# Optimization experiments

Hardware: AMD Instinct MI355X
Metric: run time of the kernel (lower is better)

The kernel has to match this reference:

```python
import jax, jax.numpy as jnp
import numpy as np

EPS = 1e-5
NUM_GRAPHS = 512


def _glorot(key, shape):
    lim = float(np.sqrt(6.0 / (shape[0] + shape[1])))
    return jax.random.uniform(key, shape, jnp.float32, -lim, lim)


def setup_inputs() -> dict:
    key = jax.random.key(0)
    ks = jax.random.split(key, 20)
    N, E, F0 = 50000, 800000, 64
    x = jax.random.normal(ks[0], (N, F0), jnp.float32)
    edge_index = jax.random.randint(ks[1], (2, E), 0, N, jnp.int64)
    batch = jnp.sort(jax.random.randint(ks[2], (N,), 0, NUM_GRAPHS, jnp.int64))
    dims = [(F0, 128), (128, 64), (64, 32)]
    p = {}
    for i, (di, do) in enumerate(dims, start=1):
        p[f"W{i}l"] = _glorot(ks[3 * i], (di, do))
        p[f"b{i}"] = jnp.zeros((do,), jnp.float32)
        p[f"W{i}r"] = _glorot(ks[3 * i + 1], (di, do))
        p[f"g{i}"] = jnp.ones((do,), jnp.float32)
        p[f"be{i}"] = jnp.zeros((do,), jnp.float32)
    p["Wf1"] = _glorot(ks[13], (32, 128)); p["bf1"] = jnp.zeros((128,), jnp.float32)
    p["Wf2"] = _glorot(ks[14], (128, 64)); p["bf2"] = jnp.zeros((64,), jnp.float32)
    p["Wf3"] = _glorot(ks[15], (64, 2)); p["bf3"] = jnp.zeros((2,), jnp.float32)
    return {"x": x, "edge_index": edge_index, "batch": batch, **p}


def _sage(x, src, dst, Wl, bl, Wr, n):
    # mean-aggregate neighbor features (gather from src, scatter-mean to dst)
    agg = jax.ops.segment_sum(x[src], dst, num_segments=n)
    cnt = jax.ops.segment_sum(jnp.ones((src.shape[0],), x.dtype), dst, num_segments=n)
    mean = agg / jnp.maximum(cnt, 1.0)[:, None]
    return mean @ Wl + bl + x @ Wr


def _bn(x, g, b):
    mu = jnp.mean(x, axis=0)
    var = jnp.mean((x - mu) ** 2, axis=0)  # biased var, torch training mode
    return (x - mu) * jax.lax.rsqrt(var + EPS) * g + b


def reference(x, edge_index, batch,
              W1l, b1, W1r, g1, be1,
              W2l, b2, W2r, g2, be2,
              W3l, b3, W3r, g3, be3,
              Wf1, bf1, Wf2, bf2, Wf3, bf3):
    n = x.shape[0]
    src, dst = edge_index[0], edge_index[1]
    h = _bn(jax.nn.relu(_sage(x, src, dst, W1l, b1, W1r, n)), g1, be1)
    h = _bn(jax.nn.relu(_sage(h, src, dst, W2l, b2, W2r, n)), g2, be2)
    h = _bn(jax.nn.relu(_sage(h, src, dst, W3l, b3, W3r, n)), g3, be3)
    pooled = jax.ops.segment_sum(h, batch, num_segments=NUM_GRAPHS)  # [G, 32]
    cr = jax.nn.relu(pooled @ Wf1 + bf1)  # dropout = identity (eval)
    cr = jax.nn.relu(cr @ Wf2 + bf2)
    cr = cr @ Wf3 + bf3
    return cr.reshape(-1, 2)
```

## Files before the change

### kernel.cpp

```cpp
#include <hip/hip_runtime.h>
#include <hip/hip_bf16.h>

#define EPSBN 1e-5f
#define NGRAPH 512
#define SCAN_NB 128
#define NXCD 8

typedef __attribute__((ext_vector_type(8))) short bf16x8;
typedef __attribute__((ext_vector_type(4))) float f32x4;

__device__ inline short f2bf(float f) {
    unsigned u = __builtin_bit_cast(unsigned, f);
    u += 0x7fffu + ((u >> 16) & 1u);
    return (short)(u >> 16);
}
__device__ inline float bf2f(short s) {
    unsigned u = ((unsigned)(unsigned short)s) << 16;
    return __builtin_bit_cast(float, u);
}

__global__ void __launch_bounds__(256) k_hist(
    const int* __restrict__ dst, int* __restrict__ hist, int E)
{
    for (int e = blockIdx.x * 256 + threadIdx.x; e < E; e += gridDim.x * 256)
        atomicAdd(&hist[dst[e]], 1);
}

__global__ void __launch_bounds__(256) k_scan1(
    const int* __restrict__ hist, int* __restrict__ blocksum, int N)
{
    __shared__ int red[256];
    const int C = (N + SCAN_NB - 1) / SCAN_NB;
    const int b = blockIdx.x, t = threadIdx.x;
    const int lo = b * C, hi = min(lo + C, N);
    int s = 0;
    for (int i = lo + t; i < hi; i += 256) s += hist[i];
    red[t] = s;
    __syncthreads();
    for (int off = 128; off; off >>= 1) {
        if (t < off) red[t] += red[t + off];
        __syncthreads();
    }
    if (t == 0) blocksum[b] = red[0];
}

__global__ void __launch_bounds__(SCAN_NB) k_scan2(
    const int* __restrict__ blocksum, int* __restrict__ blockoff,
    int* __restrict__ row_off, int N)
{
    __shared__ int tmp[SCAN_NB];
    const int t = threadIdx.x;
    int v = blocksum[t];
    tmp[t] = v;
    __syncthreads();
    for (int off = 1; off < SCAN_NB; off <<= 1) {
        int u = (t >= off) ? tmp[t - off] : 0;
        __syncthreads();
        tmp[t] += u;
        __syncthreads();
    }
    blockoff[t] = tmp[t] - v;
    if (t == SCAN_NB - 1) row_off[N] = tmp[t];
}

__global__ void __launch_bounds__(256) k_scan3(
    const int* __restrict__ hist, const int* __restrict__ blockoff,
    int* __restrict__ row_off, int* __restrict__ cursor, int N)
{
    __shared__ int red[256];
    const int C = (N + SCAN_NB - 1) / SCAN_NB;
    const int b = blockIdx.x, t = threadIdx.x;
    const int lo = b * C, hi = min(lo + C, N);
    const int TC = (C + 255) / 256;
    const int s0 = lo + t * TC;
    const int s1 = min(s0 + TC, hi);
    int s = 0;
    for (int i = s0; i < s1; i++) s += hist[i];
    red[t] = s;
    __syncthreads();
    for (int off = 1; off < 256; off <<= 1) {
        int u = (t >= off) ? red[t - off] : 0;
        __syncthreads();
        red[t] += u;
        __syncthreads();
    }
    int run = blockoff[b] + red[t] - s;
    for (int i = s0; i < s1; i++) {
        row_off[i] = run;
        cursor[i] = run;
        run += hist[i];
    }
}

__global__ void __launch_bounds__(256) k_scatter8(
    const int* __restrict__ src, const int* __restrict__ dst,
    int* __restrict__ cursor, int* __restrict__ csr, int E, int N)
{
    const int grp = blockIdx.x & (NXCD - 1);
    const int chunk = (N + NXCD - 1) / NXCD;
    const int lo = grp * chunk;
    const int hi = min(lo + chunk, N);
    const int stride = (gridDim.x >> 3) * 256;
    for (int e = (blockIdx.x >> 3) * 256 + threadIdx.x; e < E; e += stride) {
        int d = dst[e];
        if (d >= lo && d < hi) {
            int p = atomicAdd(&cursor[d], 1);
            csr[p] = src[e];
        }
    }
}

template <int F>
__global__ void __launch_bounds__(256) k_gatherb(
    const short* __restrict__ feat, const int* __restrict__ row_off,
    const int* __restrict__ csr, short* __restrict__ aggb, int N)
{
    constexpr int LPR = F / 8;
    constexpr int RPB = 256 / LPR;
    const int lane = threadIdx.x % LPR;
    const int rloc = threadIdx.x / LPR;
    for (int row = blockIdx.x * RPB + rloc; row < N; row += gridDim.x * RPB) {
        const int s0 = row_off[row];
        const int s1 = row_off[row + 1];
        float acc0[8], acc1[8];
        #pragma unroll
        for (int i = 0; i < 8; i++) { acc0[i] = 0.f; acc1[i] = 0.f; }
        int p = s0;
        for (; p + 1 < s1; p += 2) {
            int sA = csr[p];
            int sB = csr[p + 1];
            bf16x8 va = *(const bf16x8*)&feat[(long long)sA * F + lane * 8];
            bf16x8 vb = *(const bf16x8*)&feat[(long long)sB * F + lane * 8];
            #pragma unroll
            for (int i = 0; i < 8; i++) {
                acc0[i] += bf2f(va[i]);
                acc1[i] += bf2f(vb[i]);
            }
        }
        if (p < s1) {
            int sA = csr[p];
            bf16x8 va = *(const bf16x8*)&feat[(long long)sA * F + lane * 8];
            #pragma unroll
            for (int i = 0; i < 8; i++) acc0[i] += bf2f(va[i]);
        }
        short o[8];
        #pragma unroll
        for (int i = 0; i < 8; i++) o[i] = f2bf(acc0[i] + acc1[i]);
        *(bf16x8*)&aggb[(long long)row * F + lane * 8] = *(bf16x8*)o;
    }
}

__global__ void __launch_bounds__(256) k_cvt(
    const float* __restrict__ in, short* __restrict__ out, long long n4)
{
    long long i = (long long)blockIdx.x * 256 + threadIdx.x;
    if (i >= n4) return;
    float4 v = *(const float4*)&in[i * 4];
    short4 o = make_short4(f2bf(v.x), f2bf(v.y), f2bf(v.z), f2bf(v.w));
    *(short4*)&out[i * 4] = o;
}

template <int K, int F, bool AFF>
__global__ void __launch_bounds__(64) k_wprep(
    const float* __restrict__ W, const float* __restrict__ a,
    const float* __restrict__ c, const float* __restrict__ bias,
    short* __restrict__ Wt, float* __restrict__ cvec)
{
    int j = blockIdx.x * 64 + threadIdx.x;
    if (j >= F) return;
    float cv = bias ? bias[j] : 0.f;
    for (int k = 0; k < K; k++) {
        float w = W[k * F + j];
        float aa = 1.f;
        if constexpr (AFF) {
            aa = a[k];
            cv += c[k] * w;
        }
        Wt[j * K + k] = f2bf(aa * w);
    }
    cvec[j] = cv;
}

template <int K, int FOUT, bool DUAL, bool HASBASE, bool FINAL, bool OUTBF16,
          bool POOL>
__global__ void __launch_bounds__(256) k_mgemm(
    const short* __restrict__ A, const short* __restrict__ A2,
    const short* __restrict__ Wt, const short* __restrict__ Wt2,
    const float* __restrict__ cvec, const short* __restrict__ base,
    const int* __restrict__ row_off, void* outv,
    float* __restrict__ s_out, float* __restrict__ q_out,
    const int* __restrict__ batchp, float* __restrict__ praw, int N)
{
    constexpr int KS = K / 32;
    constexpr int NCT = FOUT / 16;
    const int lane = threadIdx.x & 63;
    const int wid = threadIdx.x >> 6;
    const int g = lane >> 4;
    const int mi = lane & 15;
    const int RT = (N + 15) >> 4;
    const int nw = gridDim.x * 4;
    float* outf = (float*)outv;
    short* outb = (short*)outv;

    float st_s[FINAL ? NCT : 1];
    float st_q[FINAL ? NCT : 1];
    if constexpr (FINAL) {
        #pragma unroll
        for (int ct = 0; ct < NCT; ct++) { st_s[ct] = 0.f; st_q[ct] = 0.f; }
    }

    for (int rt = blockIdx.x * 4 + wid; rt < RT; rt += nw) {
        const int m0 = rt * 16;
        int arow = m0 + mi;
        if (arow >= N) arow = N - 1;

        bf16x8 af[KS];
        bf16x8 af2[DUAL ? KS : 1];
        const short* ap = A + (long long)arow * K;
        #pragma unroll
        for (int s = 0; s < KS; s++)
            af[s] = *(const bf16x8*)(ap + s * 32 + g * 8);
        if constexpr (DUAL) {
            const short* ap2 = A2 + (long long)arow * K;
            #pragma unroll
            for (int s = 0; s < KS; s++)
                af2[s] = *(const bf16x8*)(ap2 + s * 32 + g * 8);
        }

        float invc[4];
        if constexpr (DUAL || HASBASE) {
            #pragma unroll
            for (int r = 0; r < 4; r++) {
                int row = m0 + 4 * g + r;
                int cnt = 1;
                if (row < N) cnt = max(row_off[row + 1] - row_off[row], 1);
                invc[r] = 1.f / (float)cnt;
            }
        }
        int bidx[4];
        if constexpr (POOL) {
            #pragma unroll
            for (int r = 0; r < 4; r++) {
                int row = m0 + 4 * g + r;
                bidx[r] = (row < N) ? batchp[row] : -1;
            }
        }

        #pragma unroll
        for (int ct = 0; ct < NCT; ct++) {
            f32x4 acc = {0.f, 0.f, 0.f, 0.f};
            f32x4 acc2 = {0.f, 0.f, 0.f, 0.f};
            const short* bp = Wt + (long long)(ct * 16 + mi) * K;
            #pragma unroll
            for (int s = 0; s < KS; s++) {
                bf16x8 bf = *(const bf16x8*)(bp + s * 32 + g * 8);
                acc = __builtin_amdgcn_mfma_f32_16x16x32_bf16(af[s], bf, acc, 0, 0, 0);
                if constexpr (DUAL) {
                    bf16x8 bf2 = *(const bf16x8*)(Wt2 + (long long)(ct * 16 + mi) * K + s * 32 + g * 8);
                    acc2 = __builtin_amdgcn_mfma_f32_16x16x32_bf16(af2[s], bf2, acc2, 0, 0, 0);
                }
            }
            float cv = cvec[ct * 16 + mi];
            float sl = 0.f, ql = 0.f;
            #pragma unroll
            for (int r = 0; r < 4; r++) {
                int row = m0 + 4 * g + r;
                if (row < N) {
                    float v = acc[r] + cv;
                    if constexpr (DUAL) v = fmaf(invc[r], acc2[r], v);
                    if constexpr (HASBASE)
                        v = fmaf(invc[r], bf2f(base[(long long)row * FOUT + ct * 16 + mi]), v);
                    if constexpr (FINAL) v = fmaxf(v, 0.f);
                    if constexpr (POOL) {
                        atomicAdd(&praw[bidx[r] * FOUT + ct * 16 + mi], v);
                    } else if constexpr (OUTBF16) {
                        outb[(long long)row * FOUT + ct * 16 + mi] = f2bf(v);
                    } else {
                        outf[(long long)row * FOUT + ct * 16 + mi] = v;
                    }
                    if constexpr (FINAL) { sl += v; ql += v * v; }
                }
            }
            if constexpr (FINAL) {
                sl += __shfl_xor(sl, 16, 64);
                sl += __shfl_xor(sl, 32, 64);
                ql += __shfl_xor(ql, 16, 64);
                ql += __shfl_xor(ql, 32, 64);
                st_s[ct] += sl;
                st_q[ct] += ql;
            }
        }
    }

    if constexpr (FINAL) {
        __shared__ float redS[4][NCT][16];
        __shared__ float redQ[4][NCT][16];
        if (lane < 16) {
            #pragma unroll
            for (int ct = 0; ct < NCT; ct++) {
                redS[wid][ct][lane] = st_s[ct];
                redQ[wid][ct][lane] = st_q[ct];
            }
        }
        __syncthreads();
        if (wid == 0 && lane < 16) {
            #pragma unroll
            for (int ct = 0; ct < NCT; ct++) {
                float s = redS[0][ct][lane] + redS[1][ct][lane] +
                          redS[2][ct][lane] + redS[3][ct][lane];
                float q = redQ[0][ct][lane] + redQ[1][ct][lane] +
                          redQ[2][ct][lane] + redQ[3][ct][lane];
                atomicAdd(&s_out[ct * 16 + lane], s);
                atomicAdd(&q_out[ct * 16 + lane], q);
            }
        }
    }
}

__global__ void k_finalize(const float* __restrict__ s, const float* __restrict__ q,
                           const float* __restrict__ g, const float* __restrict__ be,
                           float* __restrict__ a, float* __restrict__ c,
                           int F, float invN)
{
    int j = threadIdx.x;
    if (j < F) {
        float mu = s[j] * invN;
        float var = q[j] * invN - mu * mu;
        float aj = g[j] / sqrtf(var + EPSBN);
        a[j] = aj;
        c[j] = be[j] - mu * aj;
    }
}

__global__ void __launch_bounds__(256) k_gcnt(
    const int* __restrict__ batch, float* __restrict__ gcnt, int N)
{
    int i = blockIdx.x * 256 + threadIdx.x;
    if (i < N) atomicAdd(&gcnt[batch[i]], 1.0f);
}

__global__ void __launch_bounds__(128) k_mlp(
    const float* __restrict__ praw, const float* __restrict__ a3,
    const float* __restrict__ c3, const float* __restrict__ gcnt,
    const float* __restrict__ Wf1, const float* __restrict__ bf1,
    const float* __restrict__ Wf2, const float* __restrict__ bf2,
    const float* __restrict__ Wf3, const float* __restrict__ bf3,
    float* __restrict__ out)
{
    __shared__ float p[32], h1[128], h2[64];
    int g = blockIdx.x, t = threadIdx.x;
    if (t < 32) p[t] = a3[t] * praw[g * 32 + t] + gcnt[g] * c3[t];
    __syncthreads();
    {
        float acc = bf1[t];
        #pragma unroll
        for (int k = 0; k < 32; k++) acc += p[k] * Wf1[k * 128 + t];
        h1[t] = fmaxf(acc, 0.f);
    }
    __syncthreads();
    if (t < 64) {
        float acc = bf2[t];
        #pragma unroll
        for (int k = 0; k < 128; k++) acc += h1[k] * Wf2[k * 64 + t];
        h2[t] = fmaxf(acc, 0.f);
    }
    __syncthreads();
    if (t < 2) {
        float acc = bf3[t];
        #pragma unroll
        for (int k = 0; k < 64; k++) acc += h2[k] * Wf3[k * 2 + t];
        out[g * 2 + t] = acc;
    }
}

extern "C" void kernel_launch(void* const* d_in, const int* in_sizes, int n_in,
                              void* d_out, int out_size, void* d_ws, size_t ws_size,
                              hipStream_t stream)
{
    const float* x     = (const float*)d_in[0];
    const int*   ei    = (const int*)d_in[1];
    const int*   batch = (const int*)d_in[2];
    const float* W1l = (const float*)d_in[3];
    const float* b1  = (const float*)d_in[4];
    const float* W1r = (const float*)d_in[5];
    const float* g1  = (const float*)d_in[6];
    const float* be1 = (const float*)d_in[7];
    const float* W2l = (const float*)d_in[8];
    const float* b2  = (const float*)d_in[9];
    const float* W2r = (const float*)d_in[10];
    const float* g2  = (const float*)d_in[11];
    const float* be2 = (const float*)d_in[12];
    const float* W3l = (const float*)d_in[13];
    const float* b3  = (const float*)d_in[14];
    const float* W3r = (const float*)d_in[15];
    const float* g3  = (const float*)d_in[16];
    const float* be3 = (const float*)d_in[17];
    const float* Wf1 = (const float*)d_in[18];
    const float* bf1 = (const float*)d_in[19];
    const float* Wf2 = (const float*)d_in[20];
    const float* bf2 = (const float*)d_in[21];
    const float* Wf3 = (const float*)d_in[22];
    const float* bf3 = (const float*)d_in[23];

    const int N = in_sizes[0] / 64;
    const int E = in_sizes[1] / 2;
    const int* src = ei;
    const int* dst = ei + E;

    char* ws = (char*)d_ws;
    size_t off = 0;
    auto alloc = [&](size_t bytes) {
        size_t o = off;
        off += (bytes + 511) & ~(size_t)511;
        return o;
    };
    const size_t o_rowoff = alloc((size_t)(N + 1) * 4);
    const size_t o_hist   = alloc((size_t)N * 4);
    const size_t o_cursor = alloc((size_t)N * 4);
    const size_t o_bsum   = alloc(SCAN_NB * 4 * 2);
    const size_t o_csr    = alloc((size_t)E * 4);
    const size_t o_zoneB  = alloc((size_t)N * 128);
    const size_t o_zoneC  = alloc((size_t)N * 128);
    const size_t o_zoneD  = alloc((size_t)N * 256);
    const size_t o_zoneE  = alloc((size_t)N * 128);
    const size_t o_praw   = alloc((size_t)NGRAPH * 32 * 4);
    const size_t o_gcnt   = alloc((size_t)NGRAPH * 4);
    const size_t o_stats  = alloc(448 * 4);
    const size_t o_aff    = alloc(448 * 4);
    const size_t o_cvec   = alloc(512 * 4);
    const size_t o_wt     = alloc((8192 * 4 + 2048 * 2) * 2);
    (void)ws_size;

    int* row_off = (int*)(ws + o_rowoff);
    int* hist    = (int*)(ws + o_hist);
    int* cursor  = (int*)(ws + o_cursor);
    int* bsum    = (int*)(ws + o_bsum);
    int* boff    = bsum + SCAN_NB;
    int* csr     = (int*)(ws + o_csr);
    short* xb   = (short*)(ws + o_zoneB);
    short* y2b  = (short*)(ws + o_zoneB);
    short* aggb = (short*)(ws + o_zoneC);
    short* t2b  = (short*)(ws + o_zoneC);
    short* t1b  = (short*)(ws + o_zoneD);
    short* y3b  = (short*)(ws + o_zoneD);
    short* m2b  = (short*)(ws + o_zoneE);
    short* m3b  = (short*)(ws + o_zoneE);
    float* praw = (float*)(ws + o_praw);
    float* gcnt = (float*)(ws + o_gcnt);
    float* s1 = (float*)(ws + o_stats);
    float* q1 = s1 + 128;
    float* s2 = q1 + 128;
    float* q2 = s2 + 64;
    float* s3 = q2 + 64;
    float* q3 = s3 + 32;
    float* a1 = (float*)(ws + o_aff);
    float* c1 = a1 + 128;
    float* a2 = c1 + 128;
    float* c2 = a2 + 64;
    float* a3 = c2 + 64;
    float* c3 = a3 + 32;
    float* cv1r = (float*)(ws + o_cvec);
    float* cvdum = cv1r + 128;
    float* cv2l = cvdum + 128;
    float* cv2r = cv2l + 64;
    float* cv3l = cv2r + 64;
    float* cv3r = cv3l + 32;
    short* W1l_t = (short*)(ws + o_wt);
    short* W1r_t = W1l_t + 8192;
    short* W2l_t = W1r_t + 8192;
    short* W2r_t = W2l_t + 8192;
    short* W3l_t = W2r_t + 8192;
    short* W3r_t = W3l_t + 2048;

    const float invN = 1.0f / (float)N;
    const int MG = 512;

    hipMemsetAsync(ws + o_hist, 0, (size_t)N * 4, stream);
    hipMemsetAsync(ws + o_stats, 0, 448 * 4, stream);
    hipMemsetAsync(ws + o_praw, 0, (size_t)NGRAPH * 32 * 4, stream);
    hipMemsetAsync(ws + o_gcnt, 0, (size_t)NGRAPH * 4, stream);

    k_hist<<<2048, 256, 0, stream>>>(dst, hist, E);
    k_scan1<<<SCAN_NB, 256, 0, stream>>>(hist, bsum, N);
    k_scan2<<<1, SCAN_NB, 0, stream>>>(bsum, boff, row_off, N);
    k_scan3<<<SCAN_NB, 256, 0, stream>>>(hist, boff, row_off, cursor, N);
    k_scatter8<<<2048, 256, 0, stream>>>(src, dst, cursor, csr, E, N);
    k_gcnt<<<(N + 255) / 256, 256, 0, stream>>>(batch, gcnt, N);

    k_cvt<<<(int)(((long long)N * 16 + 255) / 256), 256, 0, stream>>>(
        x, xb, (long long)N * 16);
    k_wprep<64, 128, false><<<2, 64, 0, stream>>>(
        W1r, nullptr, nullptr, b1, W1r_t, cv1r);
    k_wprep<64, 128, false><<<2, 64, 0, stream>>>(
        W1l, nullptr, nullptr, nullptr, W1l_t, cvdum);

    k_gatherb<64><<<(N + 31) / 32, 256, 0, stream>>>(
        xb, row_off, csr, aggb, N);
    k_mgemm<64, 128, true, false, true, true, false><<<MG, 256, 0, stream>>>(
        xb, aggb, W1r_t, W1l_t, cv1r, nullptr, row_off, t1b, s1, q1,
        nullptr, nullptr, N);
    k_finalize<<<1, 128, 0, stream>>>(s1, q1, g1, be1, a1, c1, 128, invN);

    k_wprep<128, 64, true><<<1, 64, 0, stream>>>(W2l, a1, c1, nullptr, W2l_t, cv2l);
    k_wprep<128, 64, true><<<1, 64, 0, stream>>>(W2r, a1, c1, b2, W2r_t, cv2r);
    k_mgemm<128, 64, false, false, false, true, false><<<MG, 256, 0, stream>>>(
        t1b, nullptr, W2l_t, nullptr, cv2l, nullptr, row_off, y2b,
        nullptr, nullptr, nullptr, nullptr, N);
    k_gatherb<64><<<(N + 31) / 32, 256, 0, stream>>>(
        y2b, row_off, csr, m2b, N);
    k_mgemm<128, 64, false, true, true, true, false><<<MG, 256, 0, stream>>>(
        t1b, nullptr, W2r_t, nullptr, cv2r, m2b, row_off, t2b, s2, q2,
        nullptr, nullptr, N);
    k_finalize<<<1, 64, 0, stream>>>(s2, q2, g2, be2, a2, c2, 64, invN);

    k_wprep<64, 32, true><<<1, 64, 0, stream>>>(W3l, a2, c2, nullptr, W3l_t, cv3l);
    k_wprep<64, 32, true><<<1, 64, 0, stream>>>(W3r, a2, c2, b3, W3r_t, cv3r);
    k_mgemm<64, 32, false, false, false, true, false><<<MG, 256, 0, stream>>>(
        t2b, nullptr, W3l_t, nullptr, cv3l, nullptr, row_off, y3b,
        nullptr, nullptr, nullptr, nullptr, N);
    k_gatherb<32><<<(N + 63) / 64, 256, 0, stream>>>(
        y3b, row_off, csr, m3b, N);
    k_mgemm<64, 32, false, true, true, false, true><<<MG, 256, 0, stream>>>(
        t2b, nullptr, W3r_t, nullptr, cv3r, m3b, row_off, nullptr, s3, q3,
        batch, praw, N);
    k_finalize<<<1, 32, 0, stream>>>(s3, q3, g3, be3, a3, c3, 32, invN);

    k_mlp<<<NGRAPH, 128, 0, stream>>>(praw, a3, c3, gcnt,
                                      Wf1, bf1, Wf2, bf2, Wf3, bf3,
                                      (float*)d_out);
}
```

Baseline: 343.0 us.

## Cut kernel launches, merge memsets, drop XCD-partitioned scatter, unroll gather by four

Folds graph-count atomics into the histogram kernel and removes the separate scan2 kernel by having each scan3 block sum the preceding block sums serially. The four memsets become one by placing the zeroed buffers contiguously, and paired weight-prep launches are merged into one kernel per layer. The scatter no longer partitions destinations by XCD group and each edge is processed once. The gather loop now keeps four accumulators per thread instead of two, raising memory-level parallelism at some register cost.

```diff
diff --git a/kernel.cpp b/kernel.cpp
--- a/kernel.cpp
+++ b/kernel.cpp
@@ -4,7 +4,6 @@
 #define EPSBN 1e-5f
 #define NGRAPH 512
 #define SCAN_NB 128
-#define NXCD 8
 
 typedef __attribute__((ext_vector_type(8))) short bf16x8;
 typedef __attribute__((ext_vector_type(4))) float f32x4;
@@ -20,10 +19,14 @@
 }
 
 __global__ void __launch_bounds__(256) k_hist(
-    const int* __restrict__ dst, int* __restrict__ hist, int E)
-{
-    for (int e = blockIdx.x * 256 + threadIdx.x; e < E; e += gridDim.x * 256)
+    const int* __restrict__ dst, int* __restrict__ hist,
+    const int* __restrict__ batch, float* __restrict__ gcnt, int E, int N)
+{
+    const int stride = gridDim.x * 256;
+    for (int e = blockIdx.x * 256 + threadIdx.x; e < E; e += stride)
         atomicAdd(&hist[dst[e]], 1);
+    for (int i = blockIdx.x * 256 + threadIdx.x; i < N; i += stride)
+        atomicAdd(&gcnt[batch[i]], 1.0f);
 }
 
 __global__ void __launch_bounds__(256) k_scan1(
@@ -44,33 +47,25 @@
     if (t == 0) blocksum[b] = red[0];
 }
 
-__global__ void __launch_bounds__(SCAN_NB) k_scan2(
-    const int* __restrict__ blocksum, int* __restrict__ blockoff,
-    int* __restrict__ row_off, int N)
-{
-    __shared__ int tmp[SCAN_NB];
-    const int t = threadIdx.x;
-    int v = blocksum[t];
-    tmp[t] = v;
-    __syncthreads();
-    for (int off = 1; off < SCAN_NB; off <<= 1) {
-        int u = (t >= off) ? tmp[t - off] : 0;
-        __syncthreads();
-        tmp[t] += u;
-        __syncthreads();
-    }
-    blockoff[t] = tmp[t] - v;
-    if (t == SCAN_NB - 1) row_off[N] = tmp[t];
-}
-
 __global__ void __launch_bounds__(256) k_scan3(
-    const int* __restrict__ hist, const int* __restrict__ blockoff,
+    const int* __restrict__ hist, const int* __restrict__ blocksum,
     int* __restrict__ row_off, int* __restrict__ cursor, int N)
 {
     __shared__ int red[256];
+    __shared__ int boff_s;
     const int C = (N + SCAN_NB - 1) / SCAN_NB;
     const int b = blockIdx.x, t = threadIdx.x;
     const int lo = b * C, hi = min(lo + C, N);
+    if (t == 0) {
+        int acc = 0;
+        for (int i = 0; i < b; i++) acc += blocksum[i];
+        boff_s = acc;
+        if (b == SCAN_NB - 1) {
+            int tot = acc;
+            for (int i = b; i < SCAN_NB; i++) tot += blocksum[i];
+            row_off[N] = tot;
+        }
+    }
     const int TC = (C + 255) / 256;
     const int s0 = lo + t * TC;
     const int s1 = min(s0 + TC, hi);
@@ -84,7 +79,7 @@
         red[t] += u;
         __syncthreads();
     }
-    int run = blockoff[b] + red[t] - s;
+    int run = boff_s + red[t] - s;
     for (int i = s0; i < s1; i++) {
         row_off[i] = run;
         cursor[i] = run;
@@ -92,21 +87,14 @@
     }
 }
 
-__global__ void __launch_bounds__(256) k_scatter8(
+__global__ void __launch_bounds__(256) k_scatter(
     const int* __restrict__ src, const int* __restrict__ dst,
-    int* __restrict__ cursor, int* __restrict__ csr, int E, int N)
-{
-    const int grp = blockIdx.x & (NXCD - 1);
-    const int chunk = (N + NXCD - 1) / NXCD;
-    const int lo = grp * chunk;
-    const int hi = min(lo + chunk, N);
-    const int stride = (gridDim.x >> 3) * 256;
-    for (int e = (blockIdx.x >> 3) * 256 + threadIdx.x; e < E; e += stride) {
+    int* __restrict__ cursor, int* __restrict__ csr, int E)
+{
+    for (int e = blockIdx.x * 256 + threadIdx.x; e < E; e += gridDim.x * 256) {
         int d = dst[e];
-        if (d >= lo && d < hi) {
-            int p = atomicAdd(&cursor[d], 1);
-            csr[p] = src[e];
-        }
+        int p = atomicAdd(&cursor[d], 1);
+        csr[p] = src[e];
     }
 }
 
@@ -119,33 +107,40 @@
     constexpr int RPB = 256 / LPR;
     const int lane = threadIdx.x % LPR;
     const int rloc = threadIdx.x / LPR;
+    const short* fbase = feat + lane * 8;
     for (int row = blockIdx.x * RPB + rloc; row < N; row += gridDim.x * RPB) {
         const int s0 = row_off[row];
         const int s1 = row_off[row + 1];
-        float acc0[8], acc1[8];
-        #pragma unroll
-        for (int i = 0; i < 8; i++) { acc0[i] = 0.f; acc1[i] = 0.f; }
+        float acc0[8], acc1[8], acc2[8], acc3[8];
+        #pragma unroll
+        for (int i = 0; i < 8; i++) {
+            acc0[i] = 0.f; acc1[i] = 0.f; acc2[i] = 0.f; acc3[i] = 0.f;
+        }
         int p = s0;
-        for (; p + 1 < s1; p += 2) {
-            int sA = csr[p];
-            int sB = csr[p + 1];
-            bf16x8 va = *(const bf16x8*)&feat[(long long)sA * F + lane * 8];
-            bf16x8 vb = *(const bf16x8*)&feat[(long long)sB * F + lane * 8];
+        for (; p + 3 < s1; p += 4) {
+            int sA = csr[p], sB = csr[p + 1], sC = csr[p + 2], sD = csr[p + 3];
+            bf16x8 va = *(const bf16x8*)&fbase[(long long)sA * F];
+            bf16x8 vb = *(const bf16x8*)&fbase[(long long)sB * F];
+            bf16x8 vc = *(const bf16x8*)&fbase[(long long)sC * F];
+            bf16x8 vd = *(const bf16x8*)&fbase[(long long)sD * F];
             #pragma unroll
             for (int i = 0; i < 8; i++) {
                 acc0[i] += bf2f(va[i]);
                 acc1[i] += bf2f(vb[i]);
-            }
-        }
-        if (p < s1) {
+                acc2[i] += bf2f(vc[i]);
+                acc3[i] += bf2f(vd[i]);
+            }
+        }
+        for (; p < s1; p++) {
             int sA = csr[p];
-            bf16x8 va = *(const bf16x8*)&feat[(long long)sA * F + lane * 8];
+            bf16x8 va = *(const bf16x8*)&fbase[(long long)sA * F];
             #pragma unroll
             for (int i = 0; i < 8; i++) acc0[i] += bf2f(va[i]);
         }
         short o[8];
         #pragma unroll
-        for (int i = 0; i < 8; i++) o[i] = f2bf(acc0[i] + acc1[i]);
+        for (int i = 0; i < 8; i++)
+            o[i] = f2bf((acc0[i] + acc1[i]) + (acc2[i] + acc3[i]));
         *(bf16x8*)&aggb[(long long)row * F + lane * 8] = *(bf16x8*)o;
     }
 }
@@ -161,24 +156,30 @@
 }
 
 template <int K, int F, bool AFF>
-__global__ void __launch_bounds__(64) k_wprep(
-    const float* __restrict__ W, const float* __restrict__ a,
-    const float* __restrict__ c, const float* __restrict__ bias,
-    short* __restrict__ Wt, float* __restrict__ cvec)
+__global__ void __launch_bounds__(64) k_wprep2(
+    const float* __restrict__ Wl, const float* __restrict__ Wr,
+    const float* __restrict__ a, const float* __restrict__ c,
+    const float* __restrict__ bias,
+    short* __restrict__ Wlt, short* __restrict__ Wrt,
+    float* __restrict__ cvl, float* __restrict__ cvr)
 {
     int j = blockIdx.x * 64 + threadIdx.x;
-    if (j >= F) return;
-    float cv = bias ? bias[j] : 0.f;
+    const bool second = j >= F;
+    const int jj = second ? j - F : j;
+    if (jj >= F || j >= 2 * F) return;
+    const float* W = second ? Wr : Wl;
+    short* Wt = second ? Wrt : Wlt;
+    float cv = (second && bias) ? bias[jj] : 0.f;
     for (int k = 0; k < K; k++) {
-        float w = W[k * F + j];
+        float w = W[k * F + jj];
         float aa = 1.f;
         if constexpr (AFF) {
             aa = a[k];
             cv += c[k] * w;
         }
-        Wt[j * K + k] = f2bf(aa * w);
-    }
-    cvec[j] = cv;
+        Wt[jj * K + k] = f2bf(aa * w);
+    }
+    if (second) cvr[jj] = cv; else cvl[jj] = cv;
 }
 
 template <int K, int FOUT, bool DUAL, bool HASBASE, bool FINAL, bool OUTBF16,
@@ -330,13 +331,6 @@
         a[j] = aj;
         c[j] = be[j] - mu * aj;
     }
-}
-
-__global__ void __launch_bounds__(256) k_gcnt(
-    const int* __restrict__ batch, float* __restrict__ gcnt, int N)
-{
-    int i = blockIdx.x * 256 + threadIdx.x;
-    if (i < N) atomicAdd(&gcnt[batch[i]], 1.0f);
 }
 
 __global__ void __launch_bounds__(128) k_mlp(
@@ -415,27 +409,28 @@
         return o;
     };
     const size_t o_rowoff = alloc((size_t)(N + 1) * 4);
-    const size_t o_hist   = alloc((size_t)N * 4);
     const size_t o_cursor = alloc((size_t)N * 4);
-    const size_t o_bsum   = alloc(SCAN_NB * 4 * 2);
+    const size_t o_bsum   = alloc(SCAN_NB * 4);
     const size_t o_csr    = alloc((size_t)E * 4);
     const size_t o_zoneB  = alloc((size_t)N * 128);
     const size_t o_zoneC  = alloc((size_t)N * 128);
     const size_t o_zoneD  = alloc((size_t)N * 256);
     const size_t o_zoneE  = alloc((size_t)N * 128);
-    const size_t o_praw   = alloc((size_t)NGRAPH * 32 * 4);
-    const size_t o_gcnt   = alloc((size_t)NGRAPH * 4);
-    const size_t o_stats  = alloc(448 * 4);
     const size_t o_aff    = alloc(448 * 4);
     const size_t o_cvec   = alloc(512 * 4);
     const size_t o_wt     = alloc((8192 * 4 + 2048 * 2) * 2);
+    const size_t o_zero0  = off;
+    const size_t o_hist   = alloc((size_t)N * 4);
+    const size_t o_stats  = alloc(448 * 4);
+    const size_t o_praw   = alloc((size_t)NGRAPH * 32 * 4);
+    const size_t o_gcnt   = alloc((size_t)NGRAPH * 4);
+    const size_t zero_len = off - o_zero0;
     (void)ws_size;
 
     int* row_off = (int*)(ws + o_rowoff);
     int* hist    = (int*)(ws + o_hist);
     int* cursor  = (int*)(ws + o_cursor);
     int* bsum    = (int*)(ws + o_bsum);
-    int* boff    = bsum + SCAN_NB;
     int* csr     = (int*)(ws + o_csr);
     short* xb   = (short*)(ws + o_zoneB);
     short* y2b  = (short*)(ws + o_zoneB);
@@ -459,9 +454,9 @@
     float* c2 = a2 + 64;
     float* a3 = c2 + 64;
     float* c3 = a3 + 32;
-    float* cv1r = (float*)(ws + o_cvec);
-    float* cvdum = cv1r + 128;
-    float* cv2l = cvdum + 128;
+    float* cv1l = (float*)(ws + o_cvec);
+    float* cv1r = cv1l + 128;
+    float* cv2l = cv1r + 128;
     float* cv2r = cv2l + 64;
     float* cv3l = cv2r + 64;
     float* cv3r = cv3l + 32;
@@ -475,24 +470,17 @@
     const float invN = 1.0f / (float)N;
     const int MG = 512;
 
-    hipMemsetAsync(ws + o_hist, 0, (size_t)N * 4, stream);
-    hipMemsetAsync(ws + o_stats, 0, 448 * 4, stream);
-    hipMemsetAsync(ws + o_praw, 0, (size_t)NGRAPH * 32 * 4, stream);
-    hipMemsetAsync(ws + o_gcnt, 0, (size_t)NGRAPH * 4, stream);
-
-    k_hist<<<2048, 256, 0, stream>>>(dst, hist, E);
+    hipMemsetAsync(ws + o_zero0, 0, zero_len, stream);
+
+    k_hist<<<2048, 256, 0, stream>>>(dst, hist, batch, gcnt, E, N);
     k_scan1<<<SCAN_NB, 256, 0, stream>>>(hist, bsum, N);
-    k_scan2<<<1, SCAN_NB, 0, stream>>>(bsum, boff, row_off, N);
-    k_scan3<<<SCAN_NB, 256, 0, stream>>>(hist, boff, row_off, cursor, N);
-    k_scatter8<<<2048, 256, 0, stream>>>(src, dst, cursor, csr, E, N);
-    k_gcnt<<<(N + 255) / 256, 256, 0, stream>>>(batch, gcnt, N);
+    k_scan3<<<SCAN_NB, 256, 0, stream>>>(hist, bsum, row_off, cursor, N);
+    k_scatter<<<2048, 256, 0, stream>>>(src, dst, cursor, csr, E);
 
     k_cvt<<<(int)(((long long)N * 16 + 255) / 256), 256, 0, stream>>>(
         x, xb, (long long)N * 16);
-    k_wprep<64, 128, false><<<2, 64, 0, stream>>>(
-        W1r, nullptr, nullptr, b1, W1r_t, cv1r);
-    k_wprep<64, 128, false><<<2, 64, 0, stream>>>(
-        W1l, nullptr, nullptr, nullptr, W1l_t, cvdum);
+    k_wprep2<64, 128, false><<<4, 64, 0, stream>>>(
+        W1l, W1r, nullptr, nullptr, b1, W1l_t, W1r_t, cv1l, cv1r);
 
     k_gatherb<64><<<(N + 31) / 32, 256, 0, stream>>>(
         xb, row_off, csr, aggb, N);
@@ -501,8 +489,8 @@
         nullptr, nullptr, N);
     k_finalize<<<1, 128, 0, stream>>>(s1, q1, g1, be1, a1, c1, 128, invN);
 
-    k_wprep<128, 64, true><<<1, 64, 0, stream>>>(W2l, a1, c1, nullptr, W2l_t, cv2l);
-    k_wprep<128, 64, true><<<1, 64, 0, stream>>>(W2r, a1, c1, b2, W2r_t, cv2r);
+    k_wprep2<128, 64, true><<<2, 64, 0, stream>>>(
+        W2l, W2r, a1, c1, b2, W2l_t, W2r_t, cv2l, cv2r);
     k_mgemm<128, 64, false, false, false, true, false><<<MG, 256, 0, stream>>>(
         t1b, nullptr, W2l_t, nullptr, cv2l, nullptr, row_off, y2b,
         nullptr, nullptr, nullptr, nullptr, N);
@@ -513,8 +501,8 @@
         nullptr, nullptr, N);
     k_finalize<<<1, 64, 0, stream>>>(s2, q2, g2, be2, a2, c2, 64, invN);
 
-    k_wprep<64, 32, true><<<1, 64, 0, stream>>>(W3l, a2, c2, nullptr, W3l_t, cv3l);
-    k_wprep<64, 32, true><<<1, 64, 0, stream>>>(W3r, a2, c2, b3, W3r_t, cv3r);
+    k_wprep2<64, 32, true><<<1, 64, 0, stream>>>(
+        W3l, W3r, a2, c2, b3, W3l_t, W3r_t, cv3l, cv3r);
     k_mgemm<64, 32, false, false, false, true, false><<<MG, 256, 0, stream>>>(
         t2b, nullptr, W3l_t, nullptr, cv3l, nullptr, row_off, y3b,
         nullptr, nullptr, nullptr, nullptr, N);
```

Measured after the change: 333.9 us. 1.03x faster.
